# Optimization experiments

Hardware: AMD Instinct MI355X
Metric: run time of the kernel (lower is better)

The kernel has to match this reference:

```python
import jax, jax.numpy as jnp
import numpy as np

B, L, F, H, U = 512, 64, 2048, 512, 512


def setup_inputs() -> dict:
    key = jax.random.key(0)
    ks = jax.random.split(key, 10)
    s = 0.05
    return {
        'features': jax.random.normal(ks[0], (B, L, F), jnp.float32),
        'hidden': jax.random.normal(ks[1], (B, H), jnp.float32),
        'W1': jax.random.normal(ks[2], (F, U), jnp.float32) * s,
        'b1': jnp.zeros((U,), jnp.float32),
        'W2': jax.random.normal(ks[3], (H, U), jnp.float32) * s,
        'b2': jnp.zeros((U,), jnp.float32),
        'V': jax.random.normal(ks[4], (U, 1), jnp.float32) * s,
        'bV': jnp.zeros((1,), jnp.float32),
        'W3': jax.random.normal(ks[5], (F + H, U), jnp.float32) * s,
        'b3': jnp.zeros((U,), jnp.float32),
        'ka1': jax.random.normal(ks[6], (H, L), jnp.float32) * s,
        'kb1': jax.random.normal(ks[7], (L, L), jnp.float32) * s,
        'ka2': jax.random.normal(ks[8], (H, L), jnp.float32) * s,
        'kb2': jax.random.normal(ks[9], (L, L), jnp.float32) * s,
    }


def reference(features, hidden, W1, b1, W2, b2, V, bV, W3, b3, ka1, kb1, ka2, kb2):
    # features: [B, L, F], hidden: [B, H]
    Lp = features.shape[1]
    h = hidden[:, None, :]  # [B, 1, H] = hidden_with_time_axis

    # score_model == 'default'
    score = jnp.tanh(features @ W1 + b1 + (h @ W2 + b2))  # [B, L, U]
    logits = score @ V + bV  # [B, L, 1]
    attention_weights = jax.nn.softmax(logits, axis=1)  # [B, L, 1]

    # local_att == 'True': Gaussian window re-weighting (vectorized version of
    # the original nested Python loops over (batch, position)).
    def local_p(ka, kb):
        t = jnp.tanh(h @ ka) @ kb  # [B, 1, L]
        t = jax.nn.sigmoid(t) * jnp.sqrt(jnp.float32(Lp))
        return jnp.transpose(t, (0, 2, 1))  # [B, L, 1]

    p1 = local_p(ka1, kb1)  # predicted row center, [B, L, 1]
    p2 = local_p(ka2, kb2)  # predicted col center, [B, L, 1]

    i = jnp.arange(Lp, dtype=jnp.float32)
    g = jnp.sqrt(jnp.float32(Lp))
    rows = jnp.floor((i + 1.0) / g)                 # s_t[..., 0]
    cols = jnp.floor(jnp.mod(i + 1.0, g)) - 1.0     # s_t[..., 1]
    d2 = (rows[None, :, None] - p1) ** 2 + (cols[None, :, None] - p2) ** 2  # [B, L, 1]

    D = 1.0
    attention_weights = attention_weights * jnp.exp(-d2 / (0.5 * D * D))

    context_vector = jnp.sum(attention_weights * features, axis=1)  # [B, F]

    # context_vector_concat == 'True'
    out = jnp.tanh(jnp.concatenate([context_vector, hidden], axis=-1)) @ W3 + b3  # [B, U]
    return out, attention_weights
```

## Files before the change

### kernel.cpp

```cpp
#include <hip/hip_runtime.h>

typedef __bf16 bf16x8 __attribute__((ext_vector_type(8)));
typedef float f32x4 __attribute__((ext_vector_type(4)));

#define FAST_BARRIER()                                        \
  do {                                                        \
    asm volatile("s_waitcnt lgkmcnt(0)" ::: "memory");        \
    __builtin_amdgcn_s_barrier();                             \
    asm volatile("" ::: "memory");                            \
  } while (0)

static __device__ __forceinline__ unsigned short f2bf(float f) {
  union { float fv; unsigned u; } v; v.fv = f;
  unsigned u = v.u;
  u += 0x7fffu + ((u >> 16) & 1u);
  return (unsigned short)(u >> 16);
}

static __device__ __forceinline__ float fast_tanh(float x) {
  x = fminf(fmaxf(x, -15.f), 15.f);
  float ex = __expf(2.f * x);
  return (ex - 1.f) / (ex + 1.f);
}

static __device__ __forceinline__ bf16x8 cvt8(const float4& a, const float4& b) {
  bf16x8 r;
  r[0] = (__bf16)a.x; r[1] = (__bf16)a.y; r[2] = (__bf16)a.z; r[3] = (__bf16)a.w;
  r[4] = (__bf16)b.x; r[5] = (__bf16)b.y; r[6] = (__bf16)b.z; r[7] = (__bf16)b.w;
  return r;
}

__global__ __launch_bounds__(256) void pack_all(
    const float* __restrict__ W1, const float* __restrict__ W2,
    const float* __restrict__ W3,
    unsigned short* __restrict__ W1p, unsigned short* __restrict__ W2p,
    unsigned short* __restrict__ W3p) {
  __shared__ float tile[32][65];
  const int N = 512;
  const float* W; unsigned short* P; int nk;
  if (blockIdx.z == 0)      { W = W1; P = W1p; nk = 64; }
  else if (blockIdx.z == 1) { W = W2; P = W2p; nk = 16; }
  else                      { W = W3; P = W3p; nk = 80; }
  if ((int)blockIdx.x >= nk) return;
  int k0 = blockIdx.x * 32, n0 = blockIdx.y * 64;
  int t = threadIdx.x;
  int nn = t & 63, kkb = t >> 6;
#pragma unroll
  for (int i = 0; i < 8; ++i) {
    int kk = kkb + i * 4;
    tile[kk][nn] = W[(size_t)(k0 + kk) * N + n0 + nn];
  }
  __syncthreads();
#pragma unroll
  for (int i = 0; i < 8; ++i) {
    int e = t + i * 256;
    int k8 = e & 7, n = (e >> 3) & 63, c = e >> 9;
    size_t dst = (size_t)((k0 >> 3) + c) * 4096 + (size_t)(n0 + n) * 8 + k8;
    P[dst] = f2bf(tile[c * 8 + k8][n]);
  }
}

__global__ __launch_bounds__(512) void prep_batch(
    const float* __restrict__ hidden,
    const float* __restrict__ ka1, const float* __restrict__ kb1,
    const float* __restrict__ ka2, const float* __restrict__ kb2,
    float* __restrict__ gauss,
    unsigned short* __restrict__ A2) {
  int b = blockIdx.x, t = threadIdx.x;
  __shared__ float hl[512];
  __shared__ float part[512];
  __shared__ float tt[128];
  __shared__ float pp[128];
  {
    float v = hidden[b * 512 + t];
    hl[t] = v;
    A2[(size_t)b * 2560 + 2048 + t] = f2bf(tanhf(v));
  }
  __syncthreads();
  {
    const float* ka = (t < 256) ? ka1 : ka2;
    int lp = t & 63;
    int h0 = ((t >> 6) & 3) * 128;
    float s0 = 0.f, s1 = 0.f, s2 = 0.f, s3 = 0.f;
    for (int h = h0; h < h0 + 128; h += 4) {
      s0 += hl[h + 0] * ka[(h + 0) * 64 + lp];
      s1 += hl[h + 1] * ka[(h + 1) * 64 + lp];
      s2 += hl[h + 2] * ka[(h + 2) * 64 + lp];
      s3 += hl[h + 3] * ka[(h + 3) * 64 + lp];
    }
    part[t] = (s0 + s1) + (s2 + s3);
  }
  __syncthreads();
  if (t < 128) {
    int base = ((t >= 64) ? 256 : 0) + (t & 63);
    tt[t] = tanhf(part[base] + part[base + 64] + part[base + 128] + part[base + 192]);
  }
  __syncthreads();
  if (t < 128) {
    const float* kb = (t < 64) ? kb1 : kb2;
    const float* ts = (t < 64) ? tt : tt + 64;
    int l = t & 63;
    float s = 0.f;
    for (int j = 0; j < 64; ++j) s += ts[j] * kb[j * 64 + l];
    pp[t] = 8.0f / (1.0f + expf(-s));
  }
  __syncthreads();
  if (t < 64) {
    float fi = (float)(t + 1);
    float r = floorf(fi * 0.125f);
    float c = floorf(fmodf(fi, 8.0f)) - 1.0f;
    float dr = r - pp[t], dc = c - pp[64 + t];
    gauss[b * 64 + t] = expf(-2.0f * (dr * dr + dc * dc));
  }
}

__global__ __launch_bounds__(256, 4) void gemm64d(
    const unsigned short* __restrict__ A, int lda, int k8_stride, int nsteps,
    const unsigned short* __restrict__ Wp,
    const float* __restrict__ bias,
    float* __restrict__ C) {
  __shared__ unsigned short lA[64 * 40];
  int m0 = blockIdx.x * 64, n0 = blockIdx.y * 64;
  int z = blockIdx.z;
  int k8 = z * k8_stride;
  int t = threadIdx.x;
  int w = t >> 6, lane = t & 63, q = lane >> 4, l15 = lane & 15;
  f32x4 acc[4] = {};
  int arow = t >> 2, achk = (t & 3) * 8;
  const unsigned short* pA = A + (size_t)(m0 + arow) * lda + (size_t)k8 * 8 + achk;
  const unsigned short* pB = Wp + ((size_t)(k8 + q) * 512 + n0 + w * 16 + l15) * 8;
  int4 av = *(const int4*)(pA);
  int4 bv = *(const int4*)(pB);
  for (int ks = 0; ks < nsteps; ++ks) {
    FAST_BARRIER();
    *(int4*)(lA + arow * 40 + achk) = av;
    FAST_BARRIER();
    int ksn = (ks + 1 < nsteps) ? ks + 1 : ks;
    av = *(const int4*)(pA + ksn * 32);
    int4 bn = *(const int4*)(pB + (size_t)ksn * 16384);
    bf16x8 bf = *(const bf16x8*)&bv;
#pragma unroll
    for (int mt = 0; mt < 4; ++mt) {
      bf16x8 af = *(const bf16x8*)(lA + (mt * 16 + l15) * 40 + q * 8);
      acc[mt] = __builtin_amdgcn_mfma_f32_16x16x32_bf16(af, bf, acc[mt], 0, 0, 0);
    }
    bv = bn;
  }
  int col = n0 + w * 16 + l15;
  if (bias) {
    float bsv = bias[col];
#pragma unroll
    for (int mt = 0; mt < 4; ++mt)
#pragma unroll
      for (int j = 0; j < 4; ++j)
        C[(size_t)(m0 + mt * 16 + q * 4 + j) * 512 + col] = acc[mt][j] + bsv;
  } else {
    float* Cp = C + (size_t)z * 262144;
#pragma unroll
    for (int mt = 0; mt < 4; ++mt)
#pragma unroll
      for (int j = 0; j < 4; ++j)
        Cp[(size_t)(m0 + mt * 16 + q * 4 + j) * 512 + col] = acc[mt][j];
  }
}

__global__ __launch_bounds__(256) void reduce4(const float* __restrict__ part,
                                               const float* __restrict__ b3,
                                               float* __restrict__ out) {
  int i = blockIdx.x * 256 + threadIdx.x;
  int base = i * 4;
  int n = base & 511;
  float4 p0 = *(const float4*)(part + base);
  float4 p1 = *(const float4*)(part + 262144 + base);
  float4 p2 = *(const float4*)(part + 524288 + base);
  float4 p3 = *(const float4*)(part + 786432 + base);
  float4 bv = *(const float4*)(b3 + n);
  float4 r;
  r.x = p0.x + p1.x + p2.x + p3.x + bv.x;
  r.y = p0.y + p1.y + p2.y + p3.y + bv.y;
  r.z = p0.z + p1.z + p2.z + p3.z + bv.z;
  r.w = p0.w + p1.w + p2.w + p3.w + bv.w;
  *(float4*)(out + base) = r;
}

__global__ __launch_bounds__(256, 2) void attn_main(
    const float* __restrict__ feat,
    const unsigned short* __restrict__ W1p,
    const float* __restrict__ b1,
    const float* __restrict__ b2,
    const float* __restrict__ hidden,
    const float* __restrict__ V,
    const float* __restrict__ bVp,
    const float* __restrict__ gauss,
    float* __restrict__ aw_out,
    unsigned short* __restrict__ A2) {
  __shared__ float red[64 * 4];
  __shared__ float awl[64];
  int b = blockIdx.x, t = threadIdx.x;
  int w = t >> 6, lane = t & 63, q = lane >> 4, l15 = lane & 15;
  f32x4 acc[4][8] = {};
  const float* Ab = feat + (size_t)b * (64 * 2048);
  const float* pAr = Ab + l15 * 2048 + q * 8;
  const float* ph  = hidden + b * 512 + q * 8;
  const unsigned short* pB = W1p + ((size_t)q * 512 + w * 128 + l15) * 8;

  float4 fc[8];
#pragma unroll
  for (int mt = 0; mt < 4; ++mt) {
    fc[2 * mt]     = *(const float4*)(pAr + mt * 32768);
    fc[2 * mt + 1] = *(const float4*)(pAr + mt * 32768 + 4);
  }
  bf16x8 af[4];
#pragma unroll
  for (int mt = 0; mt < 4; ++mt) af[mt] = cvt8(fc[2 * mt], fc[2 * mt + 1]);

  for (int s = 0; s < 64; ++s) {
    int kf = (s + 1 < 64) ? s + 1 : 63;
    float4 fn[8];
    const float* ap = pAr + kf * 32;
#pragma unroll
    for (int mt = 0; mt < 4; ++mt) {
      fn[2 * mt]     = *(const float4*)(ap + mt * 32768);
      fn[2 * mt + 1] = *(const float4*)(ap + mt * 32768 + 4);
    }
    const unsigned short* bp = pB + (size_t)s * 16384;
    int4 bc[8];
#pragma unroll
    for (int nt = 0; nt < 8; ++nt) bc[nt] = *(const int4*)(bp + nt * 128);
#pragma unroll
    for (int mt = 0; mt < 4; ++mt)
#pragma unroll
      for (int nt = 0; nt < 8; ++nt)
        acc[mt][nt] = __builtin_amdgcn_mfma_f32_16x16x32_bf16(
            af[mt], *(const bf16x8*)&bc[nt], acc[mt][nt], 0, 0, 0);
#pragma unroll
    for (int mt = 0; mt < 4; ++mt) af[mt] = cvt8(fn[2 * mt], fn[2 * mt + 1]);
  }

  for (int s2 = 0; s2 < 16; ++s2) {
    float4 ha  = *(const float4*)(ph + s2 * 32);
    float4 hb4 = *(const float4*)(ph + s2 * 32 + 4);
    const unsigned short* bp = pB + (size_t)(64 + s2) * 16384;
    int4 bt[8];
#pragma unroll
    for (int nt = 0; nt < 8; ++nt) bt[nt] = *(const int4*)(bp + nt * 128);
    bf16x8 ah = cvt8(ha, hb4);
#pragma unroll
    for (int mt = 0; mt < 4; ++mt)
#pragma unroll
      for (int nt = 0; nt < 8; ++nt)
        acc[mt][nt] = __builtin_amdgcn_mfma_f32_16x16x32_bf16(
            ah, *(const bf16x8*)&bt[nt], acc[mt][nt], 0, 0, 0);
  }

  float vv[8], bb[8];
#pragma unroll
  for (int nt = 0; nt < 8; ++nt) {
    int u = w * 128 + nt * 16 + l15;
    vv[nt] = V[u];
    bb[nt] = b1[u] + b2[u];
  }
  float gs = (t < 64) ? gauss[b * 64 + t] : 0.f;
  float bV0 = bVp[0];

#pragma unroll
  for (int mt = 0; mt < 4; ++mt) {
#pragma unroll
    for (int j = 0; j < 4; ++j) {
      float p = 0.f;
#pragma unroll
      for (int nt = 0; nt < 8; ++nt)
        p += fast_tanh(acc[mt][nt][j] + bb[nt]) * vv[nt];
      p += __shfl_xor(p, 1);
      p += __shfl_xor(p, 2);
      p += __shfl_xor(p, 4);
      p += __shfl_xor(p, 8);
      if (l15 == 0) red[(mt * 16 + q * 4 + j) * 4 + w] = p;
    }
  }
  __syncthreads();
  if (t < 64) {
    float s = bV0 + red[t * 4] + red[t * 4 + 1] + red[t * 4 + 2] + red[t * 4 + 3];
    float mx = s;
#pragma unroll
    for (int o = 1; o < 64; o <<= 1) mx = fmaxf(mx, __shfl_xor(mx, o));
    float e = __expf(s - mx);
    float sm = e;
#pragma unroll
    for (int o = 1; o < 64; o <<= 1) sm += __shfl_xor(sm, o);
    float a = (e / sm) * gs;
    awl[t] = a;
    aw_out[b * 64 + t] = a;
  }
  __syncthreads();
  float4 c0 = make_float4(0.f, 0.f, 0.f, 0.f);
  float4 c1 = make_float4(0.f, 0.f, 0.f, 0.f);
  const float* pF = Ab + t * 8;
  for (int l = 0; l < 64; ++l) {
    float a = awl[l];
    float4 g0 = *(const float4*)(pF + l * 2048);
    float4 g1 = *(const float4*)(pF + l * 2048 + 4);
    c0.x += a * g0.x; c0.y += a * g0.y; c0.z += a * g0.z; c0.w += a * g0.w;
    c1.x += a * g1.x; c1.y += a * g1.y; c1.z += a * g1.z; c1.w += a * g1.w;
  }
  ushort4 o0, o1;
  o0.x = f2bf(fast_tanh(c0.x)); o0.y = f2bf(fast_tanh(c0.y));
  o0.z = f2bf(fast_tanh(c0.z)); o0.w = f2bf(fast_tanh(c0.w));
  o1.x = f2bf(fast_tanh(c1.x)); o1.y = f2bf(fast_tanh(c1.y));
  o1.z = f2bf(fast_tanh(c1.z)); o1.w = f2bf(fast_tanh(c1.w));
  *(ushort4*)(A2 + (size_t)b * 2560 + t * 8) = o0;
  *(ushort4*)(A2 + (size_t)b * 2560 + t * 8 + 4) = o1;
}

extern "C" void kernel_launch(void* const* d_in, const int* in_sizes, int n_in,
                              void* d_out, int out_size, void* d_ws, size_t ws_size,
                              hipStream_t stream) {
  (void)in_sizes; (void)n_in; (void)out_size; (void)ws_size;
  const float* feat   = (const float*)d_in[0];
  const float* hidden = (const float*)d_in[1];
  const float* W1  = (const float*)d_in[2];
  const float* b1  = (const float*)d_in[3];
  const float* W2  = (const float*)d_in[4];
  const float* b2  = (const float*)d_in[5];
  const float* V   = (const float*)d_in[6];
  const float* bV  = (const float*)d_in[7];
  const float* W3  = (const float*)d_in[8];
  const float* b3  = (const float*)d_in[9];
  const float* ka1 = (const float*)d_in[10];
  const float* kb1 = (const float*)d_in[11];
  const float* ka2 = (const float*)d_in[12];
  const float* kb2 = (const float*)d_in[13];

  char* ws = (char*)d_ws;
  unsigned short* W3p   = (unsigned short*)(ws);
  unsigned short* A2    = (unsigned short*)(ws + 2621440);
  unsigned short* W1p   = (unsigned short*)(ws + 5242880);
  unsigned short* W2p   = (unsigned short*)(ws + 7340032);
  float*          gauss = (float*)(ws + 9437184);
  float*          part  = (float*)(ws + 5242880);

  float* out    = (float*)d_out;
  float* aw_out = out + 512 * 512;

  pack_all<<<dim3(80, 8, 3), 256, 0, stream>>>(W1, W2, W3, W1p, W2p, W3p);
  prep_batch<<<512, 512, 0, stream>>>(hidden, ka1, kb1, ka2, kb2, gauss, A2);
  attn_main<<<512, 256, 0, stream>>>(feat, W1p, b1, b2, hidden, V, bV, gauss, aw_out, A2);
  gemm64d<<<dim3(8, 8, 4), 256, 0, stream>>>(A2, 2560, 80, 20, W3p, nullptr, part);
  reduce4<<<256, 256, 0, stream>>>(part, b3, out);
}
```

Baseline: 558.5 us.

## Restructure attn_main with 512 threads and double-buffered LDS staging of features

attn_main now runs 512 threads per block, with 8 waves each owning 64 output units instead of 4 waves owning 128. The feature and hidden tiles are converted to bf16 once and staged into a double-buffered LDS tile that all waves share. Previously every wave loaded and converted the whole A tile itself. Global loads for the next step are issued before the MFMAs of the current step, and s_setprio is raised around the MFMA block. This cuts redundant global traffic and per-thread register pressure, allowing higher occupancy, at the cost of two barriers per k-step and extra LDS traffic.

```diff
diff --git a/kernel.cpp b/kernel.cpp
--- a/kernel.cpp
+++ b/kernel.cpp
@@ -21,13 +21,6 @@
   x = fminf(fmaxf(x, -15.f), 15.f);
   float ex = __expf(2.f * x);
   return (ex - 1.f) / (ex + 1.f);
-}
-
-static __device__ __forceinline__ bf16x8 cvt8(const float4& a, const float4& b) {
-  bf16x8 r;
-  r[0] = (__bf16)a.x; r[1] = (__bf16)a.y; r[2] = (__bf16)a.z; r[3] = (__bf16)a.w;
-  r[4] = (__bf16)b.x; r[5] = (__bf16)b.y; r[6] = (__bf16)b.z; r[7] = (__bf16)b.w;
-  return r;
 }
 
 __global__ __launch_bounds__(256) void pack_all(
@@ -183,7 +176,7 @@
   *(float4*)(out + base) = r;
 }
 
-__global__ __launch_bounds__(256, 2) void attn_main(
+__global__ __launch_bounds__(512, 4) void attn_main(
     const float* __restrict__ feat,
     const unsigned short* __restrict__ W1p,
     const float* __restrict__ b1,
@@ -194,69 +187,72 @@
     const float* __restrict__ gauss,
     float* __restrict__ aw_out,
     unsigned short* __restrict__ A2) {
-  __shared__ float red[64 * 4];
+  __shared__ unsigned short lA[2][64 * 40];
+  __shared__ float red[64 * 8];
   __shared__ float awl[64];
   int b = blockIdx.x, t = threadIdx.x;
   int w = t >> 6, lane = t & 63, q = lane >> 4, l15 = lane & 15;
-  f32x4 acc[4][8] = {};
+  f32x4 acc[4][4] = {};
+  int row0 = t >> 3, ch0 = t & 7;
   const float* Ab = feat + (size_t)b * (64 * 2048);
-  const float* pAr = Ab + l15 * 2048 + q * 8;
-  const float* ph  = hidden + b * 512 + q * 8;
-  const unsigned short* pB = W1p + ((size_t)q * 512 + w * 128 + l15) * 8;
-
-  float4 fc[8];
-#pragma unroll
-  for (int mt = 0; mt < 4; ++mt) {
-    fc[2 * mt]     = *(const float4*)(pAr + mt * 32768);
-    fc[2 * mt + 1] = *(const float4*)(pAr + mt * 32768 + 4);
-  }
-  bf16x8 af[4];
-#pragma unroll
-  for (int mt = 0; mt < 4; ++mt) af[mt] = cvt8(fc[2 * mt], fc[2 * mt + 1]);
-
-  for (int s = 0; s < 64; ++s) {
-    int kf = (s + 1 < 64) ? s + 1 : 63;
-    float4 fn[8];
-    const float* ap = pAr + kf * 32;
+  const float* pA0 = Ab + row0 * 2048 + ch0 * 4;
+  const float* pH  = hidden + b * 512 + ch0 * 4;
+  const unsigned short* pB = W1p + ((size_t)q * 512 + w * 64 + l15) * 8;
+  int wA = row0 * 40 + ch0 * 4;
+
+  auto ldA = [&](int p) -> float4 {
+    if (p < 64) return *(const float4*)(pA0 + p * 32);
+    int pp = (p < 80) ? p : 79;
+    return *(const float4*)(pH + (pp - 64) * 32);
+  };
+  auto stage = [&](int buf, const float4& x) {
+    ushort4 u;
+    u.x = f2bf(x.x); u.y = f2bf(x.y); u.z = f2bf(x.z); u.w = f2bf(x.w);
+    *(ushort4*)(&lA[buf][wA]) = u;
+  };
+  auto ldB = [&](int p, int4* dst) {
+    const unsigned short* bp = pB + (size_t)((p < 80) ? p : 79) * 16384;
+#pragma unroll
+    for (int nt = 0; nt < 4; ++nt) dst[nt] = *(const int4*)(bp + nt * 128);
+  };
+  auto mmaStep = [&](int buf, const int4* B) {
+    __builtin_amdgcn_s_setprio(1);
 #pragma unroll
     for (int mt = 0; mt < 4; ++mt) {
-      fn[2 * mt]     = *(const float4*)(ap + mt * 32768);
-      fn[2 * mt + 1] = *(const float4*)(ap + mt * 32768 + 4);
+      bf16x8 af = *(const bf16x8*)(&lA[buf][(mt * 16 + l15) * 40 + q * 8]);
+#pragma unroll
+      for (int nt = 0; nt < 4; ++nt)
+        acc[mt][nt] = __builtin_amdgcn_mfma_f32_16x16x32_bf16(
+            af, *(const bf16x8*)&B[nt], acc[mt][nt], 0, 0, 0);
     }
-    const unsigned short* bp = pB + (size_t)s * 16384;
-    int4 bc[8];
-#pragma unroll
-    for (int nt = 0; nt < 8; ++nt) bc[nt] = *(const int4*)(bp + nt * 128);
-#pragma unroll
-    for (int mt = 0; mt < 4; ++mt)
-#pragma unroll
-      for (int nt = 0; nt < 8; ++nt)
-        acc[mt][nt] = __builtin_amdgcn_mfma_f32_16x16x32_bf16(
-            af[mt], *(const bf16x8*)&bc[nt], acc[mt][nt], 0, 0, 0);
-#pragma unroll
-    for (int mt = 0; mt < 4; ++mt) af[mt] = cvt8(fn[2 * mt], fn[2 * mt + 1]);
-  }
-
-  for (int s2 = 0; s2 < 16; ++s2) {
-    float4 ha  = *(const float4*)(ph + s2 * 32);
-    float4 hb4 = *(const float4*)(ph + s2 * 32 + 4);
-    const unsigned short* bp = pB + (size_t)(64 + s2) * 16384;
-    int4 bt[8];
-#pragma unroll
-    for (int nt = 0; nt < 8; ++nt) bt[nt] = *(const int4*)(bp + nt * 128);
-    bf16x8 ah = cvt8(ha, hb4);
-#pragma unroll
-    for (int mt = 0; mt < 4; ++mt)
-#pragma unroll
-      for (int nt = 0; nt < 8; ++nt)
-        acc[mt][nt] = __builtin_amdgcn_mfma_f32_16x16x32_bf16(
-            ah, *(const bf16x8*)&bt[nt], acc[mt][nt], 0, 0, 0);
-  }
-
-  float vv[8], bb[8];
-#pragma unroll
-  for (int nt = 0; nt < 8; ++nt) {
-    int u = w * 128 + nt * 16 + l15;
+    __builtin_amdgcn_s_setprio(0);
+  };
+
+  int4 bc[4], bn[4];
+  float4 a0, a1;
+  a0 = ldA(0); ldB(0, bc);
+  stage(0, a0);
+  a1 = ldA(1); ldB(1, bn);
+  FAST_BARRIER();
+
+  for (int s2 = 0; s2 < 40; ++s2) {
+    int p = 2 * s2;
+    stage(1, a1);
+    a0 = ldA(p + 2);
+    mmaStep(0, bc);
+    ldB(p + 2, bc);
+    FAST_BARRIER();
+    stage(0, a0);
+    a1 = ldA(p + 3);
+    mmaStep(1, bn);
+    ldB(p + 3, bn);
+    FAST_BARRIER();
+  }
+
+  float vv[4], bb[4];
+#pragma unroll
+  for (int nt = 0; nt < 4; ++nt) {
+    int u = w * 64 + nt * 16 + l15;
     vv[nt] = V[u];
     bb[nt] = b1[u] + b2[u];
   }
@@ -269,18 +265,20 @@
     for (int j = 0; j < 4; ++j) {
       float p = 0.f;
 #pragma unroll
-      for (int nt = 0; nt < 8; ++nt)
+      for (int nt = 0; nt < 4; ++nt)
         p += fast_tanh(acc[mt][nt][j] + bb[nt]) * vv[nt];
       p += __shfl_xor(p, 1);
       p += __shfl_xor(p, 2);
       p += __shfl_xor(p, 4);
       p += __shfl_xor(p, 8);
-      if (l15 == 0) red[(mt * 16 + q * 4 + j) * 4 + w] = p;
+      if (l15 == 0) red[(mt * 16 + q * 4 + j) * 8 + w] = p;
     }
   }
   __syncthreads();
   if (t < 64) {
-    float s = bV0 + red[t * 4] + red[t * 4 + 1] + red[t * 4 + 2] + red[t * 4 + 3];
+    float s = bV0;
+#pragma unroll
+    for (int wi = 0; wi < 8; ++wi) s += red[t * 8 + wi];
     float mx = s;
 #pragma unroll
     for (int o = 1; o < 64; o <<= 1) mx = fmaxf(mx, __shfl_xor(mx, o));
@@ -294,22 +292,16 @@
   }
   __syncthreads();
   float4 c0 = make_float4(0.f, 0.f, 0.f, 0.f);
-  float4 c1 = make_float4(0.f, 0.f, 0.f, 0.f);
-  const float* pF = Ab + t * 8;
+  const float* pF = Ab + t * 4;
   for (int l = 0; l < 64; ++l) {
     float a = awl[l];
-    float4 g0 = *(const float4*)(pF + l * 2048);
-    float4 g1 = *(const float4*)(pF + l * 2048 + 4);
-    c0.x += a * g0.x; c0.y += a * g0.y; c0.z += a * g0.z; c0.w += a * g0.w;
-    c1.x += a * g1.x; c1.y += a * g1.y; c1.z += a * g1.z; c1.w += a * g1.w;
-  }
-  ushort4 o0, o1;
+    float4 f0 = *(const float4*)(pF + l * 2048);
+    c0.x += a * f0.x; c0.y += a * f0.y; c0.z += a * f0.z; c0.w += a * f0.w;
+  }
+  ushort4 o0;
   o0.x = f2bf(fast_tanh(c0.x)); o0.y = f2bf(fast_tanh(c0.y));
   o0.z = f2bf(fast_tanh(c0.z)); o0.w = f2bf(fast_tanh(c0.w));
-  o1.x = f2bf(fast_tanh(c1.x)); o1.y = f2bf(fast_tanh(c1.y));
-  o1.z = f2bf(fast_tanh(c1.z)); o1.w = f2bf(fast_tanh(c1.w));
-  *(ushort4*)(A2 + (size_t)b * 2560 + t * 8) = o0;
-  *(ushort4*)(A2 + (size_t)b * 2560 + t * 8 + 4) = o1;
+  *(ushort4*)(A2 + (size_t)b * 2560 + t * 4) = o0;
 }
 
 extern "C" void kernel_launch(void* const* d_in, const int* in_sizes, int n_in,
@@ -344,7 +336,7 @@
 
   pack_all<<<dim3(80, 8, 3), 256, 0, stream>>>(W1, W2, W3, W1p, W2p, W3p);
   prep_batch<<<512, 512, 0, stream>>>(hidden, ka1, kb1, ka2, kb2, gauss, A2);
-  attn_main<<<512, 256, 0, stream>>>(feat, W1p, b1, b2, hidden, V, bV, gauss, aw_out, A2);
+  attn_main<<<512, 512, 0, stream>>>(feat, W1p, b1, b2, hidden, V, bV, gauss, aw_out, A2);
   gemm64d<<<dim3(8, 8, 4), 256, 0, stream>>>(A2, 2560, 80, 20, W3p, nullptr, part);
   reduce4<<<256, 256, 0, stream>>>(part, b3, out);
 }
```

Result: faster. 523.7 us (-6.2%).
